# Kernel tuning notes

Measured on AMD Instinct MI355X. Metric: run time of the kernel, lower is better.

## Reference

```python
import jax, jax.numpy as jnp
import numpy as np

IN_FEATURES = 4096
OUT_FEATURES = 4096
NNZ = 1677722  # round(0.1 * 4096 * 4096)
N_TOKENS = 8192


def setup_inputs() -> dict:
    key = jax.random.key(0)
    k1, k2, k3, k4 = jax.random.split(key, 4)
    inputs = jax.random.normal(k1, (N_TOKENS, IN_FEATURES), dtype=jnp.float32)
    bound = 1.0 / IN_FEATURES ** 0.5
    weights = jax.random.uniform(k2, (NNZ,), minval=-bound, maxval=bound, dtype=jnp.float32)
    bias = jax.random.uniform(k3, (OUT_FEATURES,), minval=-bound, maxval=bound, dtype=jnp.float32)
    # COO indices: row (output) and col (input) indices, sampled like np.random.choice
    flat = jax.random.randint(k4, (NNZ,), 0, IN_FEATURES * OUT_FEATURES)
    row_ind = flat // IN_FEATURES
    col_ind = flat % IN_FEATURES
    indices = jnp.stack((row_ind, col_ind)).astype(jnp.int64)
    return {"inputs": inputs, "weights": weights, "bias": bias, "indices": indices}


def reference(inputs, weights, bias, indices):
    # Densify COO weight (duplicates are summed, matching torch coalesce/to_dense)
    dense_w = jnp.zeros((OUT_FEATURES, IN_FEATURES), dtype=weights.dtype)
    dense_w = dense_w.at[indices[0], indices[1]].add(weights)
    # output = (W @ x^T)^T + b  ==  x @ W^T + b
    out = jnp.einsum('ni,oi->no', inputs, dense_w) + bias
    return out
```

## Files before the change

kernel.cpp:

```cpp
#include <hip/hip_runtime.h>

#define M_TOK 8192
#define NF    4096
#define KF    4096
#define BK    64
#define NT    (KF / BK)

typedef __attribute__((ext_vector_type(8))) short bf16x8;
typedef __attribute__((ext_vector_type(4))) float f32x4;
typedef __attribute__((ext_vector_type(2))) short s16x2;

__device__ __forceinline__ unsigned short f2bf(float f) {
    unsigned u = __builtin_bit_cast(unsigned, f);
    u += 0x7FFFu + ((u >> 16) & 1u);
    return (unsigned short)(u >> 16);
}

__device__ __forceinline__ float bf2f(unsigned short b) {
    unsigned u = ((unsigned)b) << 16;
    return __builtin_bit_cast(float, u);
}

__device__ __forceinline__ void load_lds16(const unsigned short* g, unsigned short* l) {
    __builtin_amdgcn_global_load_lds(
        (const __attribute__((address_space(1))) unsigned int*)g,
        (__attribute__((address_space(3))) unsigned int*)l,
        16, 0, 0);
}

__device__ __forceinline__ void block_bar() {
    asm volatile("" ::: "memory");
    __builtin_amdgcn_s_barrier();
    asm volatile("" ::: "memory");
}

#define VMCNT(n) asm volatile("s_waitcnt vmcnt(" #n ")" ::: "memory")

__global__ void prep_zero_convx(const float4* __restrict__ X, ushort4* __restrict__ Xb,
                                uint4* __restrict__ Wb, int nx4, int nwb) {
    int i = blockIdx.x * blockDim.x + threadIdx.x;
    if (i < nwb) Wb[i] = (uint4){0u, 0u, 0u, 0u};
    if (i < nx4) {
        float4 v = X[i];
        ushort4 o;
        o.x = f2bf(v.x); o.y = f2bf(v.y); o.z = f2bf(v.z); o.w = f2bf(v.w);
        Xb[i] = o;
    }
}

__global__ void scatter_bf16(const int* __restrict__ idx, const float* __restrict__ w,
                             unsigned short* __restrict__ Wb, int nnz) {
    int t = blockIdx.x * blockDim.x + threadIdx.x;
    if (t >= nnz) return;
    int r = idx[t];
    int c = idx[nnz + t];
    size_t elem = (size_t)r * KF + c;
#if __has_builtin(__builtin_amdgcn_global_atomic_fadd_v2bf16)
    unsigned short wb = f2bf(w[t]);
    s16x2 val;
    if (elem & 1) { val[0] = 0; val[1] = (short)wb; }
    else          { val[0] = (short)wb; val[1] = 0; }
    __builtin_amdgcn_global_atomic_fadd_v2bf16(
        (__attribute__((address_space(1))) s16x2*)(Wb + (elem & ~(size_t)1)), val);
#else
    unsigned* addr = (unsigned*)(Wb + (elem & ~(size_t)1));
    float wf = w[t];
    unsigned old = __hip_atomic_load(addr, __ATOMIC_RELAXED, __HIP_MEMORY_SCOPE_AGENT), assumed;
    do {
        assumed = old;
        unsigned short cur = (elem & 1) ? (unsigned short)(assumed >> 16)
                                        : (unsigned short)(assumed & 0xffffu);
        unsigned short nw = f2bf(bf2f(cur) + wf);
        unsigned newv = (elem & 1) ? ((assumed & 0x0000ffffu) | ((unsigned)nw << 16))
                                   : ((assumed & 0xffff0000u) | (unsigned)nw);
        old = atomicCAS(addr, assumed, newv);
    } while (old != assumed);
#endif
}

__global__ __launch_bounds__(512, 2) void gemm_bt_bias(
    const unsigned short* __restrict__ A,
    const unsigned short* __restrict__ B,
    const float* __restrict__ bias,
    float* __restrict__ C)
{
    __shared__ unsigned short lds_u[65536];
    char* const ldsb = (char*)lds_u;

    const int tid  = threadIdx.x;
    const int lane = tid & 63;
    const int wave = tid >> 6;
    const int wm   = wave >> 2;
    const int wn   = wave & 3;

    const int flat = blockIdx.y * 32 + blockIdx.x;
    const int swz  = (flat & 7) * 64 + (flat >> 3);
    const int bm   = swz & 31;
    const int bn   = swz >> 5;

    f32x4 acc[8][4] = {};

    const int gc   = (lane & 3) ^ ((lane >> 3) & 3);
    const int srow = wave * 16 + (lane >> 2);
    const unsigned short* gA   = A + (size_t)(bm * 256 + srow) * KF + gc * 8;
    const unsigned short* gB   = B + (size_t)(bn * 256 + srow) * KF + gc * 8;
    const unsigned short* gAHi = gA + (size_t)128 * KF;
    const unsigned short* gBHi = gB + (size_t)128 * KF;

    unsigned short* const sdus = lds_u + wave * 512;

    const int fr    = lane & 15;
    const int quad  = lane >> 4;
    const int pos16 = (quad ^ ((fr >> 1) & 3)) << 4;
    const int rdA   = (wm * 128 + fr) * 64 + pos16;
    const int rdB   = 32768 + (wn * 64 + fr) * 64 + pos16;

#define STAGE(gp, gpHi, region, pbuf, h) do { \
    load_lds16((gp)   + (h) * 32, sdus + (((pbuf) * 65536 + (region) + (h) * 16384       ) >> 1)); \
    load_lds16((gpHi) + (h) * 32, sdus + (((pbuf) * 65536 + (region) + (h) * 16384 + 8192) >> 1)); \
} while (0)

#define RD_A4(dst, pbuf, h, i0) do { \
    _Pragma("unroll") \
    for (int _i = 0; _i < 4; ++_i) \
        dst[_i] = *(const bf16x8*)(ldsb + (pbuf) * 65536 + (h) * 16384 + rdA + ((i0) + _i) * 1024); \
} while (0)

#define RD_B4(dst, pbuf, h) do { \
    _Pragma("unroll") \
    for (int _j = 0; _j < 4; ++_j) \
        dst[_j] = *(const bf16x8*)(ldsb + (pbuf) * 65536 + (h) * 16384 + rdB + _j * 1024); \
} while (0)

#define MFMA16(i0, af, bfv) do { \
    _Pragma("unroll") \
    for (int _i = 0; _i < 4; ++_i) \
        _Pragma("unroll") \
        for (int _j = 0; _j < 4; ++_j) \
            acc[(i0) + _i][_j] = __builtin_amdgcn_mfma_f32_16x16x32_bf16(af[_i], bfv[_j], acc[(i0) + _i][_j], 0, 0, 0); \
} while (0)

    STAGE(gA, gAHi, 0,     0, 0);
    STAGE(gB, gBHi, 32768, 0, 0);
    STAGE(gA, gAHi, 0,     0, 1);
    STAGE(gB, gBHi, 32768, 0, 1);
    gA += BK; gB += BK; gAHi += BK; gBHi += BK;
    VMCNT(4);
    block_bar();

    int pb = 0;
#pragma unroll 1
    for (int t = 0; t < NT - 1; ++t) {
        const int nb = pb ^ 1;
        bf16x8 a[4], b[4];
        RD_A4(a, pb, 0, 0);
        RD_B4(b, pb, 0);
        STAGE(gA, gAHi, 0, nb, 0);
        block_bar();
        __builtin_amdgcn_s_setprio(1);
        MFMA16(0, a, b);
        __builtin_amdgcn_s_setprio(0);
        block_bar();
        RD_A4(a, pb, 0, 4);
        STAGE(gB, gBHi, 32768, nb, 0);
        block_bar();
        __builtin_amdgcn_s_setprio(1);
        MFMA16(4, a, b);
        __builtin_amdgcn_s_setprio(0);
        VMCNT(4);
        block_bar();
        RD_A4(a, pb, 1, 0);
        RD_B4(b, pb, 1);
        STAGE(gA, gAHi, 0, nb, 1);
        block_bar();
        __builtin_amdgcn_s_setprio(1);
        MFMA16(0, a, b);
        __builtin_amdgcn_s_setprio(0);
        block_bar();
        RD_A4(a, pb, 1, 4);
        STAGE(gB, gBHi, 32768, nb, 1);
        block_bar();
        __builtin_amdgcn_s_setprio(1);
        MFMA16(4, a, b);
        __builtin_amdgcn_s_setprio(0);
        VMCNT(4);
        block_bar();
        gA += BK; gB += BK; gAHi += BK; gBHi += BK;
        pb = nb;
    }

    {
        bf16x8 a[4], b[4];
        RD_A4(a, pb, 0, 0);
        RD_B4(b, pb, 0);
        MFMA16(0, a, b);
        RD_A4(a, pb, 0, 4);
        MFMA16(4, a, b);
        VMCNT(0);
        block_bar();
        RD_A4(a, pb, 1, 0);
        RD_B4(b, pb, 1);
        MFMA16(0, a, b);
        RD_A4(a, pb, 1, 4);
        MFMA16(4, a, b);
    }

#undef STAGE
#undef RD_A4
#undef RD_B4
#undef MFMA16

    const int crow = bm * 256 + wm * 128;
    const int ccol = bn * 256 + wn * 64;
    const int r_l  = quad * 4;
#pragma unroll
    for (int j = 0; j < 4; ++j) {
        int col = ccol + j * 16 + fr;
        float bv = bias[col];
#pragma unroll
        for (int i = 0; i < 8; ++i) {
#pragma unroll
            for (int r = 0; r < 4; ++r)
                C[(size_t)(crow + i * 16 + r_l + r) * NF + col] = acc[i][j][r] + bv;
        }
    }
}

extern "C" void kernel_launch(void* const* d_in, const int* in_sizes, int n_in,
                              void* d_out, int out_size, void* d_ws, size_t ws_size,
                              hipStream_t stream) {
    const float* x    = (const float*)d_in[0];
    const float* w    = (const float*)d_in[1];
    const float* bias = (const float*)d_in[2];
    const int*   idx  = (const int*)d_in[3];
    float* out = (float*)d_out;
    const int nnz = in_sizes[1];

    unsigned short* Wb = (unsigned short*)d_ws;
    unsigned short* Xb = (unsigned short*)((char*)d_ws + (size_t)NF * KF * sizeof(unsigned short));

    const int nx4 = M_TOK * KF / 4;
    const int nwb = NF * KF * 2 / 16;

    prep_zero_convx<<<(nx4 + 255) / 256, 256, 0, stream>>>(
        (const float4*)x, (ushort4*)Xb, (uint4*)Wb, nx4, nwb);
    scatter_bf16<<<(nnz + 255) / 256, 256, 0, stream>>>(idx, w, Wb, nnz);
    gemm_bt_bias<<<dim3(32, 16), 512, 0, stream>>>(Xb, Wb, bias, out);
}
```

Measured before the change: 554.0 us.

## Restructure GEMM mainloop into four-stage half-tile ring buffer and remap tile swizzle

Replaces the double-buffered BK=64 mainloop with a 4-slot ring of 32-wide K sub-tiles in the same 128KB LDS, keeping three sub-tiles in flight ahead of compute. The goal is to hide global-to-LDS latency more deeply. The block-to-tile mapping also changes so that each XCD gets an 8x8 square patch of output tiles, which should improve L2 reuse of A and B. In exchange there are more barriers per unit of K and an unrolled epilogue with hardcoded slot offsets, which must match the ring indices exactly.

```diff
diff --git a/kernel.cpp b/kernel.cpp
--- a/kernel.cpp
+++ b/kernel.cpp
@@ -4,7 +4,7 @@
 #define NF    4096
 #define KF    4096
 #define BK    64
-#define NT    (KF / BK)
+#define NHALF 128
 
 typedef __attribute__((ext_vector_type(8))) short bf16x8;
 typedef __attribute__((ext_vector_type(4))) float f32x4;
@@ -94,9 +94,10 @@
     const int wn   = wave & 3;
 
     const int flat = blockIdx.y * 32 + blockIdx.x;
-    const int swz  = (flat & 7) * 64 + (flat >> 3);
-    const int bm   = swz & 31;
-    const int bn   = swz >> 5;
+    const int xcd  = flat & 7;
+    const int q    = flat >> 3;
+    const int bm   = (xcd & 3) * 8 + (q & 7);
+    const int bn   = (xcd >> 2) * 8 + (q >> 3);
 
     f32x4 acc[8][4] = {};
 
@@ -107,29 +108,33 @@
     const unsigned short* gAHi = gA + (size_t)128 * KF;
     const unsigned short* gBHi = gB + (size_t)128 * KF;
 
-    unsigned short* const sdus = lds_u + wave * 512;
+    unsigned short* const sd = lds_u + wave * 512;
 
     const int fr    = lane & 15;
     const int quad  = lane >> 4;
     const int pos16 = (quad ^ ((fr >> 1) & 3)) << 4;
     const int rdA   = (wm * 128 + fr) * 64 + pos16;
-    const int rdB   = 32768 + (wn * 64 + fr) * 64 + pos16;
-
-#define STAGE(gp, gpHi, region, pbuf, h) do { \
-    load_lds16((gp)   + (h) * 32, sdus + (((pbuf) * 65536 + (region) + (h) * 16384       ) >> 1)); \
-    load_lds16((gpHi) + (h) * 32, sdus + (((pbuf) * 65536 + (region) + (h) * 16384 + 8192) >> 1)); \
-} while (0)
-
-#define RD_A4(dst, pbuf, h, i0) do { \
+    const int rdB   = 16384 + (wn * 64 + fr) * 64 + pos16;
+
+#define STAGE_A(sb, ko) do { \
+    load_lds16(gA   + (ko), sd + (((sb)        ) >> 1)); \
+    load_lds16(gAHi + (ko), sd + (((sb) +  8192) >> 1)); \
+} while (0)
+#define STAGE_B(sb, ko) do { \
+    load_lds16(gB   + (ko), sd + (((sb) + 16384) >> 1)); \
+    load_lds16(gBHi + (ko), sd + (((sb) + 24576) >> 1)); \
+} while (0)
+
+#define RD_A4(dst, sb, i0) do { \
     _Pragma("unroll") \
     for (int _i = 0; _i < 4; ++_i) \
-        dst[_i] = *(const bf16x8*)(ldsb + (pbuf) * 65536 + (h) * 16384 + rdA + ((i0) + _i) * 1024); \
-} while (0)
-
-#define RD_B4(dst, pbuf, h) do { \
+        dst[_i] = *(const bf16x8*)(ldsb + (sb) + rdA + ((i0) + _i) * 1024); \
+} while (0)
+
+#define RD_B4(dst, sb) do { \
     _Pragma("unroll") \
     for (int _j = 0; _j < 4; ++_j) \
-        dst[_j] = *(const bf16x8*)(ldsb + (pbuf) * 65536 + (h) * 16384 + rdB + _j * 1024); \
+        dst[_j] = *(const bf16x8*)(ldsb + (sb) + rdB + _j * 1024); \
 } while (0)
 
 #define MFMA16(i0, af, bfv) do { \
@@ -140,72 +145,68 @@
             acc[(i0) + _i][_j] = __builtin_amdgcn_mfma_f32_16x16x32_bf16(af[_i], bfv[_j], acc[(i0) + _i][_j], 0, 0, 0); \
 } while (0)
 
-    STAGE(gA, gAHi, 0,     0, 0);
-    STAGE(gB, gBHi, 32768, 0, 0);
-    STAGE(gA, gAHi, 0,     0, 1);
-    STAGE(gB, gBHi, 32768, 0, 1);
-    gA += BK; gB += BK; gAHi += BK; gBHi += BK;
-    VMCNT(4);
+    STAGE_A(0, 0);       STAGE_B(0, 0);
+    STAGE_A(32768, 32);  STAGE_B(32768, 32);
+    STAGE_A(65536, 64);  STAGE_B(65536, 64);
+    VMCNT(8);
     block_bar();
 
-    int pb = 0;
+    int ko3 = 96;
 #pragma unroll 1
-    for (int t = 0; t < NT - 1; ++t) {
-        const int nb = pb ^ 1;
+    for (int g = 0; g < NHALF - 3; ++g) {
+        const int sb  = (g & 3) << 15;
+        const int sbn = ((g + 3) & 3) << 15;
         bf16x8 a[4], b[4];
-        RD_A4(a, pb, 0, 0);
-        RD_B4(b, pb, 0);
-        STAGE(gA, gAHi, 0, nb, 0);
+        RD_A4(a, sb, 0);
+        RD_B4(b, sb);
+        STAGE_A(sbn, ko3);
         block_bar();
         __builtin_amdgcn_s_setprio(1);
         MFMA16(0, a, b);
         __builtin_amdgcn_s_setprio(0);
         block_bar();
-        RD_A4(a, pb, 0, 4);
-        STAGE(gB, gBHi, 32768, nb, 0);
+        RD_A4(a, sb, 4);
+        STAGE_B(sbn, ko3);
         block_bar();
         __builtin_amdgcn_s_setprio(1);
         MFMA16(4, a, b);
         __builtin_amdgcn_s_setprio(0);
-        VMCNT(4);
-        block_bar();
-        RD_A4(a, pb, 1, 0);
-        RD_B4(b, pb, 1);
-        STAGE(gA, gAHi, 0, nb, 1);
-        block_bar();
-        __builtin_amdgcn_s_setprio(1);
-        MFMA16(0, a, b);
-        __builtin_amdgcn_s_setprio(0);
-        block_bar();
-        RD_A4(a, pb, 1, 4);
-        STAGE(gB, gBHi, 32768, nb, 1);
-        block_bar();
-        __builtin_amdgcn_s_setprio(1);
-        MFMA16(4, a, b);
-        __builtin_amdgcn_s_setprio(0);
-        VMCNT(4);
-        block_bar();
-        gA += BK; gB += BK; gAHi += BK; gBHi += BK;
-        pb = nb;
+        VMCNT(8);
+        block_bar();
+        ko3 += 32;
     }
 
     {
         bf16x8 a[4], b[4];
-        RD_A4(a, pb, 0, 0);
-        RD_B4(b, pb, 0);
-        MFMA16(0, a, b);
-        RD_A4(a, pb, 0, 4);
+        RD_A4(a, 32768, 0);
+        RD_B4(b, 32768);
+        block_bar();
+        MFMA16(0, a, b);
+        block_bar();
+        RD_A4(a, 32768, 4);
+        block_bar();
+        MFMA16(4, a, b);
+        VMCNT(4);
+        block_bar();
+        RD_A4(a, 65536, 0);
+        RD_B4(b, 65536);
+        block_bar();
+        MFMA16(0, a, b);
+        block_bar();
+        RD_A4(a, 65536, 4);
+        block_bar();
         MFMA16(4, a, b);
         VMCNT(0);
         block_bar();
-        RD_A4(a, pb, 1, 0);
-        RD_B4(b, pb, 1);
-        MFMA16(0, a, b);
-        RD_A4(a, pb, 1, 4);
-        MFMA16(4, a, b);
-    }
-
-#undef STAGE
+        RD_A4(a, 98304, 0);
+        RD_B4(b, 98304);
+        MFMA16(0, a, b);
+        RD_A4(a, 98304, 4);
+        MFMA16(4, a, b);
+    }
+
+#undef STAGE_A
+#undef STAGE_B
 #undef RD_A4
 #undef RD_B4
 #undef MFMA16
```

Measured after the change: 537.4 us. 3.0% less time.
